# Kernel optimization log

Hardware: AMD Instinct MI355X
Metric: run time of the kernel (lower is better)

## Reference

```python
import jax, jax.numpy as jnp
import numpy as np

B, N_VIS, N_TOT, D, H, DEPTH = 4, 512, 2048, 768, 8, 2
HID = 3072  # int(D * 4.0)
TOKEN_DIM = 768


def setup_inputs() -> dict:
    key = jax.random.key(0)
    ks = jax.random.split(key, 20)
    s = 0.02
    # mask: exactly N_VIS True per row (visible positions), random placement
    u = jax.random.uniform(ks[0], (B, N_TOT))
    rank = jnp.argsort(jnp.argsort(u, axis=1), axis=1)
    mask = rank < N_VIS
    inp = {
        'visible_tokens': jax.random.normal(ks[1], (B, N_VIS, D), jnp.float32),
        'mask': mask,
        'mask_token': jax.random.normal(ks[2], (D,), jnp.float32) * s,
        'gamma1': jnp.ones((DEPTH, D), jnp.float32),
        'beta1': jnp.zeros((DEPTH, D), jnp.float32),
        'Wqkv': jax.random.normal(ks[3], (DEPTH, 3 * D, D), jnp.float32) * s,
        'bqkv': jnp.zeros((DEPTH, 3 * D), jnp.float32),
        'Wo': jax.random.normal(ks[4], (DEPTH, D, D), jnp.float32) * s,
        'bo': jnp.zeros((DEPTH, D), jnp.float32),
        'gamma2': jnp.ones((DEPTH, D), jnp.float32),
        'beta2': jnp.zeros((DEPTH, D), jnp.float32),
        'W1': jax.random.normal(ks[5], (DEPTH, HID, D), jnp.float32) * s,
        'b1': jnp.zeros((DEPTH, HID), jnp.float32),
        'W2': jax.random.normal(ks[6], (DEPTH, D, HID), jnp.float32) * s,
        'b2': jnp.zeros((DEPTH, D), jnp.float32),
        'gn': jnp.ones((D,), jnp.float32),
        'gb': jnp.zeros((D,), jnp.float32),
        'Wdec': jax.random.normal(ks[7], (TOKEN_DIM, D), jnp.float32) * s,
        'bdec': jnp.zeros((TOKEN_DIM,), jnp.float32),
    }
    return inp


def layer_norm(x, g, b, eps=1e-5):
    mu = jnp.mean(x, axis=-1, keepdims=True)
    var = jnp.var(x, axis=-1, keepdims=True)
    return (x - mu) * jax.lax.rsqrt(var + eps) * g + b


def mha(x, Wqkv, bqkv, Wo, bo):
    Bq, N, Dm = x.shape
    dh = Dm // H
    qkv = x @ Wqkv.T + bqkv  # (B,N,3D)
    q, k, v = jnp.split(qkv, 3, axis=-1)
    q = q.reshape(Bq, N, H, dh).transpose(0, 2, 1, 3)
    k = k.reshape(Bq, N, H, dh).transpose(0, 2, 1, 3)
    v = v.reshape(Bq, N, H, dh).transpose(0, 2, 1, 3)
    scores = jnp.einsum('bhqd,bhkd->bhqk', q, k) / jnp.sqrt(jnp.float32(dh))
    attn = jax.nn.softmax(scores, axis=-1)
    out = jnp.einsum('bhqk,bhkd->bhqd', attn, v)
    out = out.transpose(0, 2, 1, 3).reshape(Bq, N, Dm)
    return out @ Wo.T + bo


def decoder_block(x, g1, be1, Wqkv, bqkv, Wo, bo, g2, be2, W1f, b1f, W2f, b2f):
    x = x + mha(layer_norm(x, g1, be1), Wqkv, bqkv, Wo, bo)
    h = layer_norm(x, g2, be2)
    h = jax.nn.gelu(h @ W1f.T + b1f, approximate=False)
    return x + h @ W2f.T + b2f


def reference(visible_tokens, mask, mask_token, gamma1, beta1, Wqkv, bqkv, Wo, bo,
              gamma2, beta2, W1, b1, W2, b2, gn, gb, Wdec, bdec):
    # Vectorized in-order scatter: position n gets visible token #(count of True in mask[:, :n+1]) - 1
    idx = jnp.clip(jnp.cumsum(mask.astype(jnp.int32), axis=1) - 1, 0, N_VIS - 1)  # (B, N_TOT)
    gathered = jnp.take_along_axis(visible_tokens, idx[..., None], axis=1)  # (B, N_TOT, D)
    x = jnp.where(mask[..., None], gathered, mask_token)
    for i in range(DEPTH):
        x = decoder_block(x, gamma1[i], beta1[i], Wqkv[i], bqkv[i], Wo[i], bo[i],
                          gamma2[i], beta2[i], W1[i], b1[i], W2[i], b2[i])
    x = layer_norm(x, gn, gb)
    return x @ Wdec.T + bdec  # (B, N_TOT, token_dim)
```

## Files before the change

### kernel.cpp

```cpp
#include <hip/hip_runtime.h>
#include <stdint.h>

typedef __attribute__((ext_vector_type(8))) __bf16 bf16x8;
typedef __attribute__((ext_vector_type(4))) float f32x4;

#define DEVI static __device__ __forceinline__

#define QK_SCALE 0.10206207261596577f

DEVI uint16_t f2bf(float f){
  union{float f; uint32_t u;} v; v.f=f;
  uint32_t u = v.u;
  uint32_t r = u + 0x7FFFu + ((u>>16)&1u);
  return (uint16_t)(r>>16);
}
DEVI void gload16(const void* g, void* l){
  __builtin_amdgcn_global_load_lds((const __attribute__((address_space(1))) unsigned int*)g,
                                   (__attribute__((address_space(3))) unsigned int*)l, 16, 0, 0);
}
template<int N> DEVI void waitvm(){
  if constexpr(N>=8)      asm volatile("s_waitcnt vmcnt(8)" ::: "memory");
  else if constexpr(N==6) asm volatile("s_waitcnt vmcnt(6)" ::: "memory");
  else if constexpr(N==4) asm volatile("s_waitcnt vmcnt(4)" ::: "memory");
  else if constexpr(N==3) asm volatile("s_waitcnt vmcnt(3)" ::: "memory");
  else                    asm volatile("s_waitcnt vmcnt(0)" ::: "memory");
}
DEVI float gelu_fast(float x){
  float x3 = x*x*x;
  float z2 = 1.5957691216f*x + 0.0713548162f*x3;
  return x / (1.0f + __expf(-z2));
}


__global__ void cvt4_f32_bf16(const float* __restrict__ a, int na, uint16_t* __restrict__ oa,
                              const float* __restrict__ b, int nb, uint16_t* __restrict__ ob,
                              const float* __restrict__ c, int nc, uint16_t* __restrict__ oc,
                              const float* __restrict__ d, int nd, uint16_t* __restrict__ od){
  int total = na+nb+nc+nd;
  int stride = gridDim.x*blockDim.x;
  for(int i = blockIdx.x*blockDim.x + threadIdx.x; i<total; i+=stride){
    int j = i;
    if(j < na){ oa[j] = f2bf(a[j]); continue; }
    j -= na;
    if(j < nb){ ob[j] = f2bf(b[j]); continue; }
    j -= nb;
    if(j < nc){ oc[j] = f2bf(c[j]); continue; }
    j -= nc;
    od[j] = f2bf(d[j]);
  }
}

__global__ __launch_bounds__(256) void cvt_wqkv(const float* __restrict__ in, uint16_t* __restrict__ out){
  int r = blockIdx.x;
  int rr = (r >= 2304) ? r - 2304 : r;
  float s = (rr < 768) ? QK_SCALE : 1.0f;
  const float* src = in + (size_t)r*768;
  uint16_t* dst = out + (size_t)r*768;
  int t = threadIdx.x;
  dst[t]     = f2bf(src[t]*s);
  dst[t+256] = f2bf(src[t+256]*s);
  dst[t+512] = f2bf(src[t+512]*s);
}

__global__ void scale_bqkv(const float* __restrict__ in, float* __restrict__ out){
  int i = blockIdx.x*blockDim.x + threadIdx.x;
  if(i < 2*2304){
    float v = in[i];
    if((i % 2304) < 768) v *= QK_SCALE;
    out[i] = v;
  }
}

__global__ void detect_mask(const uint8_t* __restrict__ mask, int* __restrict__ flag){
  __shared__ int cnt;
  if(threadIdx.x==0) cnt=0;
  __syncthreads();
  int c=0;
  for(int i=threadIdx.x;i<2048;i+=blockDim.x) c += (mask[i]!=0) ? 1 : 0;
  atomicAdd(&cnt, c);
  __syncthreads();
  if(threadIdx.x==0) *flag = (cnt==512) ? 1 : 0;
}

__global__ void scatter_idx(const void* __restrict__ maskp, const int* __restrict__ flag,
                            int* __restrict__ idx, uint8_t* __restrict__ mb){
  int b = blockIdx.x;
  int t = threadIdx.x;
  int f = *flag;
  const uint8_t* m8  = (const uint8_t*)maskp + (size_t)b*2048;
  const int*     m32 = (const int*)maskp + (size_t)b*2048;
  int v[8]; int s=0;
  for(int j=0;j<8;j++){ int n=t*8+j; int mv = f ? (m8[n]!=0) : (m32[n]!=0); v[j]=mv; s+=mv; }
  __shared__ int ps[256];
  ps[t]=s; __syncthreads();
  int acc=0;
  for(int i=0;i<t;i++) acc += ps[i];
  int cum=acc;
  for(int j=0;j<8;j++){
    int n=t*8+j;
    cum += v[j];
    int id = cum-1; id = id<0?0:(id>511?511:id);
    idx[(size_t)b*2048+n]=id;
    mb[(size_t)b*2048+n]=(uint8_t)v[j];
  }
}

__global__ void build_x(const float* __restrict__ vis, const float* __restrict__ mtok,
                        const int* __restrict__ idx, const uint8_t* __restrict__ mb,
                        float* __restrict__ x){
  int bn = blockIdx.x;
  int b = bn>>11;
  int id = idx[bn]; int m = mb[bn];
  const float* src = m ? (vis + ((size_t)b*512 + id)*768) : mtok;
  float* dst = x + (size_t)bn*768;
  for(int d=threadIdx.x; d<768; d+=256) dst[d] = src[d];
}

__global__ __launch_bounds__(256) void ln_kernel(const float* __restrict__ x,
                const float* __restrict__ g, const float* __restrict__ be,
                uint16_t* __restrict__ out){
  int w = threadIdx.x >> 6, l = threadIdx.x & 63;
  int row = blockIdx.x*4 + w;
  const float* xr = x + (size_t)row*768;
  float4 a[3];
  #pragma unroll
  for(int j=0;j<3;j++) a[j] = *(const float4*)(xr + l*4 + j*256);
  float s=0.f, q=0.f;
  #pragma unroll
  for(int j=0;j<3;j++){
    s += a[j].x+a[j].y+a[j].z+a[j].w;
    q += a[j].x*a[j].x + a[j].y*a[j].y + a[j].z*a[j].z + a[j].w*a[j].w;
  }
  #pragma unroll
  for(int off=32; off>0; off>>=1){ s+=__shfl_xor(s,off,64); q+=__shfl_xor(q,off,64); }
  float mean = s*(1.f/768.f);
  float var  = q*(1.f/768.f) - mean*mean;
  float rstd = rsqrtf(var + 1e-5f);
  uint16_t* orow = out + (size_t)row*768;
  #pragma unroll
  for(int j=0;j<3;j++){
    int col = l*4 + j*256;
    float4 gv = *(const float4*)(g + col);
    float4 bv = *(const float4*)(be + col);
    ushort4 o;
    o.x = f2bf((a[j].x-mean)*rstd*gv.x + bv.x);
    o.y = f2bf((a[j].y-mean)*rstd*gv.y + bv.y);
    o.z = f2bf((a[j].z-mean)*rstd*gv.z + bv.z);
    o.w = f2bf((a[j].w-mean)*rstd*gv.w + bv.w);
    *(ushort4*)(orow + col) = o;
  }
}

__global__ __launch_bounds__(128) void vtrans_kernel(const uint16_t* __restrict__ qkv,
                                                     uint16_t* __restrict__ vt){
  int nc = blockIdx.x, bh = blockIdx.y;
  int b = bh >> 3, h = bh & 7;
  int d = threadIdx.x;
  if(d >= 96) return;
  const uint16_t* src = qkv + ((size_t)(b*2048 + nc*8))*2304 + 1536 + h*96 + d;
  uint16_t vbuf[8];
  #pragma unroll
  for(int j=0;j<8;j++) vbuf[j] = src[(size_t)j*2304];
  *(uint4*)&vt[((size_t)bh*96 + d)*2048 + nc*8] = *(const uint4*)vbuf;
}

template<int BM, int BN, int WGM, int WGN, int GELU, int OUTF32, int PAIRED>
__global__ __launch_bounds__(WGM*WGN*64) void gemm_kernel(const uint16_t* __restrict__ A,
        const uint16_t* __restrict__ W, const float* __restrict__ bias,
        const float* __restrict__ resid, void* __restrict__ outp,
        int M, int N, int K){
  constexpr int THREADS = WGM*WGN*64;
  constexpr int WTM = BM/WGM, WTN = BN/WGN;
  constexpr int MFM = WTM/16, MFN = WTN/16;
  constexpr int NCA = BM*4/THREADS;
  constexpr int NCB = BN*4/THREADS;
  constexpr int PT  = NCA + NCB;
  constexpr int NBUF = PAIRED ? 4 : 3;
  __shared__ uint16_t sA[NBUF][BM*32];
  __shared__ uint16_t sB[NBUF][BN*32];
  int tid = threadIdx.x;
  int l = tid & 63, w = tid >> 6;
  int row0 = blockIdx.x*BM, col0 = blockIdx.y*BN;
  int wm = w / WGN, wn = w % WGN;
  f32x4 zero = {0.f,0.f,0.f,0.f};
  f32x4 acc[MFM][MFN];
  #pragma unroll
  for(int m=0;m<MFM;m++)
    #pragma unroll
    for(int n=0;n<MFN;n++) acc[m][n]=zero;
  int lr = l&15;
  int q4 = l>>4;
  int nkt = K >> 5;

  int jperm = (l&3) ^ ((l>>3)&3);
  const uint16_t* gaP[NCA]; int ldsA[NCA];
  const uint16_t* gbP[NCB]; int ldsB[NCB];
  #pragma unroll
  for(int c=0;c<NCA;c++){
    int cb = c*THREADS + w*64;
    gaP[c] = A + (size_t)(row0 + (cb>>2) + (l>>2))*K + jperm*8;
    ldsA[c] = cb*16;
  }
  #pragma unroll
  for(int c=0;c<NCB;c++){
    int cb = c*THREADS + w*64;
    gbP[c] = W + (size_t)(col0 + (cb>>2) + (l>>2))*K + jperm*8;
    ldsB[c] = cb*16;
  }
  auto stage = [&](int ktile, int b){
    int k0 = ktile*32;
    #pragma unroll
    for(int c=0;c<NCA;c++) gload16(gaP[c] + k0, (char*)sA[b] + ldsA[c]);
    #pragma unroll
    for(int c=0;c<NCB;c++) gload16(gbP[c] + k0, (char*)sB[b] + ldsB[c]);
  };

  int rdoff = (lr*4 + (q4 ^ ((lr>>1)&3)))*8;

  auto compute = [&](int b){
    const uint16_t* pA = sA[b];
    const uint16_t* pB = sB[b];
    bf16x8 af[MFM], bfr[MFN];
    #pragma unroll
    for(int m=0;m<MFM;m++) af[m]  = *(const bf16x8*)(pA + (wm*(WTM/16) + m)*512 + rdoff);
    #pragma unroll
    for(int n=0;n<MFN;n++) bfr[n] = *(const bf16x8*)(pB + (wn*(WTN/16) + n)*512 + rdoff);
    __builtin_amdgcn_s_setprio(1);
    #pragma unroll
    for(int m=0;m<MFM;m++)
      #pragma unroll
      for(int n=0;n<MFN;n++)
        acc[m][n] = __builtin_amdgcn_mfma_f32_16x16x32_bf16(af[m], bfr[n], acc[m][n], 0,0,0);
    __builtin_amdgcn_s_setprio(0);
  };

  if constexpr(PAIRED){
    stage(0, 0); stage(1, 1);
    int cur = 0;
    for(int kt=0; kt<nkt; kt+=2){
      if(kt > 0) __builtin_amdgcn_s_barrier();
      if(kt+2 < nkt){ stage(kt+2, 2*(cur^1)); stage(kt+3, 2*(cur^1)+1); }
      if(kt+2 < nkt) waitvm<2*PT>();
      else           waitvm<0>();
      __builtin_amdgcn_s_barrier();
      __builtin_amdgcn_sched_barrier(0);
      compute(2*cur);
      compute(2*cur+1);
      cur ^= 1;
    }
  } else {
    stage(0, 0);
    if(nkt > 1) stage(1, 1);
    int cur = 0;
    for(int kt=0; kt<nkt; kt++){
      if(kt > 0) __builtin_amdgcn_s_barrier();
      if(kt+2 < nkt){
        int nb = cur+2; if(nb>=3) nb-=3;
        stage(kt+2, nb);
      }
      if(kt+2 < nkt)      waitvm<2*PT>();
      else if(kt+1 < nkt) waitvm<PT>();
      else                waitvm<0>();
      __builtin_amdgcn_s_barrier();
      __builtin_amdgcn_sched_barrier(0);
      compute(cur);
      cur = (cur==2) ? 0 : cur+1;
    }
  }
  #pragma unroll
  for(int m=0;m<MFM;m++){
    int r0 = row0 + wm*WTM + m*16 + (l>>4)*4;
    #pragma unroll
    for(int n=0;n<MFN;n++){
      int cc = col0 + wn*WTN + n*16 + lr;
      float bv = bias[cc];
      #pragma unroll
      for(int i=0;i<4;i++){
        int r = r0+i;
        float v = acc[m][n][i] + bv;
        if(GELU) v = gelu_fast(v);
        if(resid) v += resid[(size_t)r*N + cc];
        if(OUTF32) ((float*)outp)[(size_t)r*N + cc] = v;
        else ((uint16_t*)outp)[(size_t)r*N + cc] = f2bf(v);
      }
    }
  }
}

__global__ __launch_bounds__(512) void attn_kernel(const uint16_t* __restrict__ qkv,
                                                   const uint16_t* __restrict__ vt,
                                                   uint16_t* __restrict__ out){
  int qt = blockIdx.x, bh = blockIdx.y;
  int b = bh >> 3, h = bh & 7;
  int tid = threadIdx.x, l = tid&63, w = tid>>6;
  __shared__ union ShMem {
    uint16_t Qs[128*104];
    struct { uint16_t K[2][64*128]; uint16_t V[2][96*64]; uint16_t Ps[128*72]; } s;
  } sh;
  const size_t rs = 2304;
  const uint16_t* qbase = qkv + ((size_t)(b*2048 + qt*128))*rs + h*96;
  const uint16_t* kbase = qkv + ((size_t)(b*2048))*rs + 768 + h*96;
  const uint16_t* vbase = vt + (size_t)bh*96*2048;

  #pragma unroll
  for(int it=0; it<3; it++){
    int c = it*512 + tid;
    int r = c/12, col = (c%12)*8;
    *(uint4*)&sh.Qs[r*104 + col] = *(const uint4*)(qbase + (size_t)r*rs + col);
  }
  __syncthreads();
  int lr = l&15, lk = (l>>4)*8;
  bf16x8 qf[3];
  #pragma unroll
  for(int ks=0;ks<3;ks++) qf[ks] = *(const bf16x8*)(sh.Qs + (w*16+lr)*104 + ks*32 + lk);
  __syncthreads();

  int ck1 = w*64 + l, ck2 = 512 + w*64 + l;
  int kr1 = ck1>>4, ks1 = ck1&15, kj1 = ks1 ^ (kr1&15); if(kj1>=12) kj1=0;
  int kr2 = ck2>>4, ks2 = ck2&15, kj2 = ks2 ^ (kr2&15); if(kj2>=12) kj2=0;
  const uint16_t* kp1 = kbase + (size_t)kr1*rs + kj1*8;
  const uint16_t* kp2 = kbase + (size_t)kr2*rs + kj2*8;
  int kl1 = (w*64)*16, kl2 = (512 + w*64)*16;
  int cv1 = w*64 + l;
  int vd1 = cv1>>3, vs1 = cv1&7, vj1 = vs1 ^ (vd1&7);
  const uint16_t* vp1 = vbase + (size_t)vd1*2048 + vj1*8;
  int vl1 = (w*64)*16;
  int cv2 = 512 + ((w&3)*64) + l;
  int vd2 = cv2>>3, vs2 = cv2&7, vj2 = vs2 ^ (vd2&7);
  const uint16_t* vp2 = vbase + (size_t)vd2*2048 + vj2*8;
  int vl2 = (512 + (w&3)*64)*16;

  auto dmaKV = [&](int buf){
    char* kb0 = (char*)sh.s.K[buf];
    char* vb0 = (char*)sh.s.V[buf];
    gload16(kp1, kb0 + kl1);
    gload16(kp2, kb0 + kl2);
    gload16(vp1, vb0 + vl1);
    if(w < 4) gload16(vp2, vb0 + vl2);
    kp1 += (size_t)64*rs; kp2 += (size_t)64*rs; vp1 += 64; vp2 += 64;
  };

  float l_run[4];
  f32x4 zero = {0.f,0.f,0.f,0.f};
  f32x4 accO[6];
  #pragma unroll
  for(int i=0;i<4;i++) l_run[i]=0.f;
  #pragma unroll
  for(int d=0;d<6;d++) accO[d]=zero;

  dmaKV(0);
  int cur = 0;
  for(int kt=0; kt<32; kt++){
    if(kt > 0) __builtin_amdgcn_s_barrier();
    if(kt+1 < 32){
      dmaKV(cur^1);
      if(w < 4) asm volatile("s_waitcnt vmcnt(4)" ::: "memory");
      else      asm volatile("s_waitcnt vmcnt(3)" ::: "memory");
    } else {
      asm volatile("s_waitcnt vmcnt(0)" ::: "memory");
    }
    __builtin_amdgcn_s_barrier();
    __builtin_amdgcn_sched_barrier(0);

    const uint16_t* Kc = sh.s.K[cur];
    const uint16_t* Vc = sh.s.V[cur];
    f32x4 accS[4];
    #pragma unroll
    for(int nf=0;nf<4;nf++) accS[nf]=zero;
    __builtin_amdgcn_s_setprio(1);
    #pragma unroll
    for(int ks=0;ks<3;ks++){
      bf16x8 q = qf[ks];
      #pragma unroll
      for(int nf=0;nf<4;nf++){
        int slot = (ks*4 + (l>>4)) ^ lr;
        bf16x8 kf = *(const bf16x8*)(Kc + (nf*16+lr)*128 + slot*8);
        accS[nf] = __builtin_amdgcn_mfma_f32_16x16x32_bf16(q, kf, accS[nf], 0,0,0);
      }
    }
    __builtin_amdgcn_s_setprio(0);
    #pragma unroll
    for(int i=0;i<4;i++){
      float ps = 0.f;
      #pragma unroll
      for(int nf=0;nf<4;nf++){
        float p = __expf(accS[nf][i]);
        ps += p;
        union{float f; uint32_t u;} pv; pv.f = p;
        sh.s.Ps[(w*16 + (l>>4)*4 + i)*72 + nf*16 + lr] = (uint16_t)(pv.u >> 16);
      }
      l_run[i] += ps;
    }
    __builtin_amdgcn_s_setprio(1);
    #pragma unroll
    for(int c2=0;c2<2;c2++){
      bf16x8 pf = *(const bf16x8*)(sh.s.Ps + (w*16+lr)*72 + c2*32 + lk);
      #pragma unroll
      for(int d=0;d<6;d++){
        int slot = (c2*4 + (l>>4)) ^ (lr&7);
        bf16x8 vf = *(const bf16x8*)(Vc + (d*16+lr)*64 + slot*8);
        accO[d] = __builtin_amdgcn_mfma_f32_16x16x32_bf16(pf, vf, accO[d], 0,0,0);
      }
    }
    __builtin_amdgcn_s_setprio(0);
    cur ^= 1;
  }
  float rl[4];
  #pragma unroll
  for(int i=0;i<4;i++){
    float s = l_run[i];
    #pragma unroll
    for(int off=1;off<16;off<<=1) s += __shfl_xor(s, off, 64);
    rl[i] = 1.0f / s;
  }
  uint16_t* obase = out + ((size_t)(b*2048 + qt*128 + w*16))*768 + h*96;
  #pragma unroll
  for(int d=0;d<6;d++){
    #pragma unroll
    for(int i=0;i<4;i++){
      int r = (l>>4)*4 + i;
      obase[(size_t)r*768 + d*16 + lr] = f2bf(accO[d][i] * rl[i]);
    }
  }
}


extern "C" void kernel_launch(void* const* d_in, const int* in_sizes, int n_in,
                              void* d_out, int out_size, void* d_ws, size_t ws_size,
                              hipStream_t stream){
  const float* vis   = (const float*)d_in[0];
  const void*  mask  = d_in[1];
  const float* mtok  = (const float*)d_in[2];
  const float* gamma1= (const float*)d_in[3];
  const float* beta1 = (const float*)d_in[4];
  const float* Wqkv  = (const float*)d_in[5];
  const float* bqkv  = (const float*)d_in[6];
  const float* Wo    = (const float*)d_in[7];
  const float* bo    = (const float*)d_in[8];
  const float* gamma2= (const float*)d_in[9];
  const float* beta2 = (const float*)d_in[10];
  const float* W1    = (const float*)d_in[11];
  const float* b1    = (const float*)d_in[12];
  const float* W2    = (const float*)d_in[13];
  const float* b2    = (const float*)d_in[14];
  const float* gn    = (const float*)d_in[15];
  const float* gb    = (const float*)d_in[16];
  const float* Wdec  = (const float*)d_in[17];
  const float* bdec  = (const float*)d_in[18];

  char* ws = (char*)d_ws;
  size_t off = 0;
  auto alloc = [&](size_t bytes)->void*{
    void* p = ws + off; off = (off + bytes + 255) & ~(size_t)255; return p;
  };
  int*      flag = (int*)alloc(4);
  int*      idx  = (int*)alloc(8192*4);
  uint8_t*  mb   = (uint8_t*)alloc(8192);
  float*    sbq  = (float*)alloc(2*2304*4);
  float*    x    = (float*)alloc((size_t)8192*768*4);
  uint16_t* lnb  = (uint16_t*)alloc((size_t)8192*768*2);
  uint16_t* qkvb = (uint16_t*)alloc((size_t)8192*3072*2);
  uint16_t* wq   = (uint16_t*)alloc((size_t)2*2304*768*2);
  uint16_t* wo   = (uint16_t*)alloc((size_t)2*768*768*2);
  uint16_t* w1   = (uint16_t*)alloc((size_t)2*3072*768*2);
  uint16_t* w2   = (uint16_t*)alloc((size_t)2*768*3072*2);
  uint16_t* wd   = (uint16_t*)alloc((size_t)768*768*2);
  uint16_t* vtb  = qkvb + (size_t)8192*2304;

  cvt_wqkv<<<4608,256,0,stream>>>(Wqkv, wq);
  scale_bqkv<<<18,256,0,stream>>>(bqkv, sbq);
  cvt4_f32_bf16<<<1024,256,0,stream>>>(Wo, 2*768*768, wo,
                                       W1, 2*3072*768, w1,
                                       W2, 2*768*3072, w2,
                                       Wdec, 768*768, wd);

  detect_mask<<<1,256,0,stream>>>((const uint8_t*)mask, flag);
  scatter_idx<<<4,256,0,stream>>>(mask, flag, idx, mb);
  build_x<<<8192,256,0,stream>>>(vis, mtok, idx, mb, x);

  for(int i=0;i<2;i++){
    ln_kernel<<<2048,256,0,stream>>>(x, gamma1+i*768, beta1+i*768, lnb);
    gemm_kernel<128,128,2,2,0,0,0><<<dim3(64,18),256,0,stream>>>(lnb, wq+(size_t)i*2304*768, sbq+i*2304,
                                                   nullptr, qkvb, 8192, 2304, 768);
    vtrans_kernel<<<dim3(256,32),128,0,stream>>>(qkvb, vtb);
    attn_kernel<<<dim3(16,32),512,0,stream>>>(qkvb, vtb, lnb);
    gemm_kernel<128,64,2,2,0,1,1><<<dim3(64,12),256,0,stream>>>(lnb, wo+(size_t)i*768*768, bo+i*768,
                                                  x, x, 8192, 768, 768);
    ln_kernel<<<2048,256,0,stream>>>(x, gamma2+i*768, beta2+i*768, lnb);
    gemm_kernel<128,128,2,2,1,0,0><<<dim3(64,24),256,0,stream>>>(lnb, w1+(size_t)i*3072*768, b1+i*3072,
                                                   nullptr, qkvb, 8192, 3072, 768);
    gemm_kernel<128,64,2,2,0,1,1><<<dim3(64,12),256,0,stream>>>(qkvb, w2+(size_t)i*768*3072, b2+i*768,
                                                  x, x, 8192, 768, 3072);
  }
  ln_kernel<<<2048,256,0,stream>>>(x, gn, gb, lnb);
  gemm_kernel<128,64,2,2,0,1,1><<<dim3(64,12),256,0,stream>>>(lnb, wd, bdec, nullptr, d_out, 8192, 768, 768);
}
```

Baseline: 628.3 us.

## Fuse V transpose into QKV GEMM epilogue and merge small setup kernels

The QKV projection GEMM epilogue now also writes the V columns in transposed per-head layout, which removes the separate vtrans kernel and its extra read of the V slice. The bias scaling is folded into the weight-conversion kernel as extra blocks, and the mask-type detection is folded into scatter_idx, cutting three small launches. In exchange, the V-column GEMM tiles do scattered 8-byte stores into the transposed buffer, and each scatter block recounts the mask.

```diff
diff --git a/kernel.cpp b/kernel.cpp
--- a/kernel.cpp
+++ b/kernel.cpp
@@ -50,45 +50,42 @@
   }
 }
 
-__global__ __launch_bounds__(256) void cvt_wqkv(const float* __restrict__ in, uint16_t* __restrict__ out){
+__global__ __launch_bounds__(256) void cvt_wqkv(const float* __restrict__ in, uint16_t* __restrict__ out,
+                                                const float* __restrict__ bin, float* __restrict__ bout){
   int r = blockIdx.x;
+  int t = threadIdx.x;
+  if(r >= 4608){
+    int i = (r-4608)*256 + t;
+    if(i < 2*2304){
+      float v = bin[i];
+      if((i % 2304) < 768) v *= QK_SCALE;
+      bout[i] = v;
+    }
+    return;
+  }
   int rr = (r >= 2304) ? r - 2304 : r;
   float s = (rr < 768) ? QK_SCALE : 1.0f;
   const float* src = in + (size_t)r*768;
   uint16_t* dst = out + (size_t)r*768;
-  int t = threadIdx.x;
   dst[t]     = f2bf(src[t]*s);
   dst[t+256] = f2bf(src[t+256]*s);
   dst[t+512] = f2bf(src[t+512]*s);
 }
 
-__global__ void scale_bqkv(const float* __restrict__ in, float* __restrict__ out){
-  int i = blockIdx.x*blockDim.x + threadIdx.x;
-  if(i < 2*2304){
-    float v = in[i];
-    if((i % 2304) < 768) v *= QK_SCALE;
-    out[i] = v;
-  }
-}
-
-__global__ void detect_mask(const uint8_t* __restrict__ mask, int* __restrict__ flag){
-  __shared__ int cnt;
-  if(threadIdx.x==0) cnt=0;
-  __syncthreads();
-  int c=0;
-  for(int i=threadIdx.x;i<2048;i+=blockDim.x) c += (mask[i]!=0) ? 1 : 0;
-  atomicAdd(&cnt, c);
-  __syncthreads();
-  if(threadIdx.x==0) *flag = (cnt==512) ? 1 : 0;
-}
-
-__global__ void scatter_idx(const void* __restrict__ maskp, const int* __restrict__ flag,
+__global__ void scatter_idx(const void* __restrict__ maskp,
                             int* __restrict__ idx, uint8_t* __restrict__ mb){
   int b = blockIdx.x;
   int t = threadIdx.x;
-  int f = *flag;
   const uint8_t* m8  = (const uint8_t*)maskp + (size_t)b*2048;
   const int*     m32 = (const int*)maskp + (size_t)b*2048;
+  __shared__ int cnt;
+  if(t==0) cnt=0;
+  __syncthreads();
+  int c=0;
+  for(int i=t;i<2048;i+=256) c += (m8[i]!=0) ? 1 : 0;
+  atomicAdd(&cnt, c);
+  __syncthreads();
+  int f = (cnt==512) ? 1 : 0;
   int v[8]; int s=0;
   for(int j=0;j<8;j++){ int n=t*8+j; int mv = f ? (m8[n]!=0) : (m32[n]!=0); v[j]=mv; s+=mv; }
   __shared__ int ps[256];
@@ -151,23 +148,11 @@
   }
 }
 
-__global__ __launch_bounds__(128) void vtrans_kernel(const uint16_t* __restrict__ qkv,
-                                                     uint16_t* __restrict__ vt){
-  int nc = blockIdx.x, bh = blockIdx.y;
-  int b = bh >> 3, h = bh & 7;
-  int d = threadIdx.x;
-  if(d >= 96) return;
-  const uint16_t* src = qkv + ((size_t)(b*2048 + nc*8))*2304 + 1536 + h*96 + d;
-  uint16_t vbuf[8];
-  #pragma unroll
-  for(int j=0;j<8;j++) vbuf[j] = src[(size_t)j*2304];
-  *(uint4*)&vt[((size_t)bh*96 + d)*2048 + nc*8] = *(const uint4*)vbuf;
-}
-
-template<int BM, int BN, int WGM, int WGN, int GELU, int OUTF32, int PAIRED>
+template<int BM, int BN, int WGM, int WGN, int GELU, int OUTF32, int PAIRED, int VT>
 __global__ __launch_bounds__(WGM*WGN*64) void gemm_kernel(const uint16_t* __restrict__ A,
         const uint16_t* __restrict__ W, const float* __restrict__ bias,
         const float* __restrict__ resid, void* __restrict__ outp,
+        uint16_t* __restrict__ vt,
         int M, int N, int K){
   constexpr int THREADS = WGM*WGN*64;
   constexpr int WTM = BM/WGM, WTN = BN/WGN;
@@ -274,6 +259,7 @@
     for(int n=0;n<MFN;n++){
       int cc = col0 + wn*WTN + n*16 + lr;
       float bv = bias[cc];
+      uint16_t cb16[4];
       #pragma unroll
       for(int i=0;i<4;i++){
         int r = r0+i;
@@ -281,7 +267,20 @@
         if(GELU) v = gelu_fast(v);
         if(resid) v += resid[(size_t)r*N + cc];
         if(OUTF32) ((float*)outp)[(size_t)r*N + cc] = v;
-        else ((uint16_t*)outp)[(size_t)r*N + cc] = f2bf(v);
+        else {
+          uint16_t h = f2bf(v);
+          cb16[i] = h;
+          ((uint16_t*)outp)[(size_t)r*N + cc] = h;
+        }
+      }
+      if constexpr(VT){
+        if(cc >= 1536){
+          int dfull = cc - 1536;
+          int bh = (r0 >> 11)*8 + dfull/96;
+          int dd = dfull % 96;
+          ushort4 pv; pv.x = cb16[0]; pv.y = cb16[1]; pv.z = cb16[2]; pv.w = cb16[3];
+          *(ushort4*)&vt[((size_t)bh*96 + dd)*2048 + (r0 & 2047)] = pv;
+        }
       }
     }
   }
@@ -453,7 +452,6 @@
   auto alloc = [&](size_t bytes)->void*{
     void* p = ws + off; off = (off + bytes + 255) & ~(size_t)255; return p;
   };
-  int*      flag = (int*)alloc(4);
   int*      idx  = (int*)alloc(8192*4);
   uint8_t*  mb   = (uint8_t*)alloc(8192);
   float*    sbq  = (float*)alloc(2*2304*4);
@@ -467,31 +465,28 @@
   uint16_t* wd   = (uint16_t*)alloc((size_t)768*768*2);
   uint16_t* vtb  = qkvb + (size_t)8192*2304;
 
-  cvt_wqkv<<<4608,256,0,stream>>>(Wqkv, wq);
-  scale_bqkv<<<18,256,0,stream>>>(bqkv, sbq);
+  cvt_wqkv<<<4626,256,0,stream>>>(Wqkv, wq, bqkv, sbq);
   cvt4_f32_bf16<<<1024,256,0,stream>>>(Wo, 2*768*768, wo,
                                        W1, 2*3072*768, w1,
                                        W2, 2*768*3072, w2,
                                        Wdec, 768*768, wd);
 
-  detect_mask<<<1,256,0,stream>>>((const uint8_t*)mask, flag);
-  scatter_idx<<<4,256,0,stream>>>(mask, flag, idx, mb);
+  scatter_idx<<<4,256,0,stream>>>(mask, idx, mb);
   build_x<<<8192,256,0,stream>>>(vis, mtok, idx, mb, x);
 
   for(int i=0;i<2;i++){
     ln_kernel<<<2048,256,0,stream>>>(x, gamma1+i*768, beta1+i*768, lnb);
-    gemm_kernel<128,128,2,2,0,0,0><<<dim3(64,18),256,0,stream>>>(lnb, wq+(size_t)i*2304*768, sbq+i*2304,
-                                                   nullptr, qkvb, 8192, 2304, 768);
-    vtrans_kernel<<<dim3(256,32),128,0,stream>>>(qkvb, vtb);
+    gemm_kernel<128,128,2,2,0,0,0,1><<<dim3(64,18),256,0,stream>>>(lnb, wq+(size_t)i*2304*768, sbq+i*2304,
+                                                   nullptr, qkvb, vtb, 8192, 2304, 768);
     attn_kernel<<<dim3(16,32),512,0,stream>>>(qkvb, vtb, lnb);
-    gemm_kernel<128,64,2,2,0,1,1><<<dim3(64,12),256,0,stream>>>(lnb, wo+(size_t)i*768*768, bo+i*768,
-                                                  x, x, 8192, 768, 768);
+    gemm_kernel<128,64,2,2,0,1,1,0><<<dim3(64,12),256,0,stream>>>(lnb, wo+(size_t)i*768*768, bo+i*768,
+                                                  x, x, nullptr, 8192, 768, 768);
     ln_kernel<<<2048,256,0,stream>>>(x, gamma2+i*768, beta2+i*768, lnb);
-    gemm_kernel<128,128,2,2,1,0,0><<<dim3(64,24),256,0,stream>>>(lnb, w1+(size_t)i*3072*768, b1+i*3072,
-                                                   nullptr, qkvb, 8192, 3072, 768);
-    gemm_kernel<128,64,2,2,0,1,1><<<dim3(64,12),256,0,stream>>>(qkvb, w2+(size_t)i*768*3072, b2+i*768,
-                                                  x, x, 8192, 768, 3072);
+    gemm_kernel<128,128,2,2,1,0,0,0><<<dim3(64,24),256,0,stream>>>(lnb, w1+(size_t)i*3072*768, b1+i*3072,
+                                                   nullptr, qkvb, nullptr, 8192, 3072, 768);
+    gemm_kernel<128,64,2,2,0,1,1,0><<<dim3(64,12),256,0,stream>>>(qkvb, w2+(size_t)i*768*3072, b2+i*768,
+                                                  x, x, nullptr, 8192, 768, 3072);
   }
   ln_kernel<<<2048,256,0,stream>>>(x, gn, gb, lnb);
-  gemm_kernel<128,64,2,2,0,1,1><<<dim3(64,12),256,0,stream>>>(lnb, wd, bdec, nullptr, d_out, 8192, 768, 768);
-}
+  gemm_kernel<128,64,2,2,0,1,1,0><<<dim3(64,12),256,0,stream>>>(lnb, wd, bdec, nullptr, d_out, nullptr, 8192, 768, 768);
+}
```

After: 611.2 us (median of 2 runs). 1.03x faster.
